# Performance work log

Hardware: AMD Instinct MI355X
Metric: run time of the kernel (lower is better)

Reference implementation:

```python
import jax, jax.numpy as jnp
from jax import lax
import numpy as np

NUM_TAGS = 64
B, T = 1024, 512


def setup_inputs() -> dict:
    key = jax.random.key(0)
    k1, k2, k3, k4, k5 = jax.random.split(key, 5)
    emissions = jax.random.normal(k1, (B, T, NUM_TAGS), dtype=jnp.float32)
    mask = jnp.ones((B, T), dtype=bool)
    tags = jax.random.randint(k2, (B, T), 0, NUM_TAGS, dtype=jnp.int32)
    # torch init: uniform(-0.1, 0.1)
    start_transitions = jax.random.uniform(k3, (NUM_TAGS,), jnp.float32, -0.1, 0.1)
    transitions = jax.random.uniform(k4, (NUM_TAGS, NUM_TAGS), jnp.float32, -0.1, 0.1)
    end_transitions = jax.random.uniform(k5, (NUM_TAGS,), jnp.float32, -0.1, 0.1)
    return {
        "emissions": emissions,
        "mask": mask,
        "tags": tags,
        "start_transitions": start_transitions,
        "transitions": transitions,
        "end_transitions": end_transitions,
    }


def _crf_nll(emissions, mask, tags, start_transitions, transitions, end_transitions):
    # emissions [B,T,K], mask [B,T] bool, tags [B,T] int
    em = jnp.moveaxis(emissions, 1, 0)        # [T,B,K]
    msk = jnp.moveaxis(mask, 1, 0)            # [T,B]
    tg = jnp.moveaxis(tags, 1, 0)             # [T,B]

    alpha0 = start_transitions[None, :] + em[0]   # [B,K]

    # ---- log-partition: logsumexp forward recursion ----
    def step_z(alpha, inp):
        e_t, m_t = inp
        # sum over previous tag i: alpha[b,i] + transitions[i,j]
        res = jax.nn.logsumexp(alpha[:, :, None] + transitions[None, :, :], axis=1)
        alpha = jnp.where(m_t[:, None], res + e_t, alpha)
        return alpha, None

    alphaT, _ = lax.scan(step_z, alpha0, (em[1:], msk[1:]))
    z = jax.nn.logsumexp(alphaT + end_transitions[None, :], axis=-1)  # [B]

    # ---- posterior (gold-path) potential recursion ----
    def step_p(beta, inp):
        e_t, m_t, prev_tag = inp
        prev_score = jnp.take_along_axis(beta, prev_tag[:, None], axis=1)  # [B,1]
        res = transitions[prev_tag] + prev_score                           # [B,K]
        beta = jnp.where(m_t[:, None], res + e_t, beta)
        return beta, None

    betaT, _ = lax.scan(step_p, alpha0, (em[1:], msk[1:], tg[:-1]))
    last_idx = jnp.sum(mask, axis=1) - 1                                    # [B]
    tag_last = jnp.take_along_axis(tags, last_idx[:, None], axis=1)[:, 0]   # [B]
    path_score = (jnp.take_along_axis(betaT, tag_last[:, None], axis=1)[:, 0]
                  + end_transitions[tag_last])                               # [B]

    nll = path_score - z
    return jnp.mean(nll)  # reduction='mean'


def reference(emissions, mask, tags, start_transitions, transitions, end_transitions):
    return _crf_nll(emissions, mask, tags, start_transitions, transitions, end_transitions)
```

## Files before the change

### kernel.cpp

```cpp
#include <hip/hip_runtime.h>


#define KTAGS 64
#define TSEQ 512
#define BATCH 1024
#define WPB 4

__global__ __launch_bounds__(256, 1) void crf_nll_kernel(
    const float* __restrict__ emissions,
    const int*   __restrict__ tags,
    const float* __restrict__ start_t,
    const float* __restrict__ trans,
    const float* __restrict__ end_t,
    float* __restrict__ out)
{
    __shared__ float trans_lds[KTAGS * KTAGS];
    __shared__ __align__(16) float q_lds[WPB][KTAGS];
    __shared__ int tags_lds[WPB][TSEQ];

    const int tid  = threadIdx.x;
    const int lane = tid & 63;
    const int wid  = tid >> 6;
    const int b    = blockIdx.x * WPB + wid;

    for (int i = tid; i < KTAGS * KTAGS; i += 256) trans_lds[i] = trans[i];
    const int* tag_row = tags + b * TSEQ;
    for (int i = lane; i < TSEQ; i += 64) tags_lds[wid][i] = tag_row[i];
    __syncthreads();

    float Ereg[KTAGS];
#pragma unroll
    for (int i = 0; i < KTAGS; ++i) Ereg[i] = __expf(trans[i * KTAGS + lane]);

    const float* em_row = emissions + (size_t)b * TSEQ * KTAGS;

    float e0     = em_row[lane];
    float alpha0 = start_t[lane] + e0;
    float beta   = alpha0;
    float c      = __shfl(alpha0, 0);
    float C      = c;
    float q      = __expf(alpha0 - c);
    q_lds[wid][lane] = q;

    float e_cur = em_row[1 * KTAGS + lane];
    float e_nxt = em_row[2 * KTAGS + lane];
    float pf0   = em_row[3 * KTAGS + lane];
    float pf1   = em_row[4 * KTAGS + lane];
    float pf2   = em_row[5 * KTAGS + lane];
    float e0c   = __shfl(e_cur, 0);
    float wc    = __expf(e_cur - e0c);

#pragma unroll 4
    for (int t = 1; t < TSEQ; ++t) {
        int   idx   = t + 5 < TSEQ ? t + 5 : TSEQ - 1;
        float e_new = em_row[idx * KTAGS + lane];

        float e0n = __shfl(e_nxt, 0);
        float wn  = __expf(e_nxt - e0n);

        const float4* pv4 = (const float4*)q_lds[wid];
        float4 qv[KTAGS / 4];
#pragma unroll
        for (int i = 0; i < KTAGS / 4; ++i) qv[i] = pv4[i];

        float a0 = 0.f, a1 = 0.f, a2 = 0.f, a3 = 0.f;
#pragma unroll
        for (int i = 0; i < KTAGS / 4; ++i) {
            a0 = fmaf(qv[i].x, Ereg[4 * i + 0], a0);
            a1 = fmaf(qv[i].y, Ereg[4 * i + 1], a1);
            a2 = fmaf(qv[i].z, Ereg[4 * i + 2], a2);
            a3 = fmaf(qv[i].w, Ereg[4 * i + 3], a3);
        }
        float s = (a0 + a1) + (a2 + a3);

        float sf   = __shfl(s, 0);
        float rinv = __builtin_amdgcn_rcpf(sf);
        C += __logf(sf) + e0c;
        q = s * rinv * wc;

        int   pt = tags_lds[wid][t - 1];
        float bp = __shfl(beta, pt);
        beta = trans_lds[pt * KTAGS + lane] + bp + e_cur;

        q_lds[wid][lane] = q;

        e_cur = e_nxt; e0c = e0n; wc = wn;
        e_nxt = pf0; pf0 = pf1; pf1 = pf2; pf2 = e_new;
    }

    float v  = q * __expf(end_t[lane]);
    float se = v;
#pragma unroll
    for (int off = 32; off > 0; off >>= 1) se += __shfl_xor(se, off);
    float z = C + __logf(se);

    int   tl   = tags_lds[wid][TSEQ - 1];
    float bl   = __shfl(beta, tl);
    float path = bl + end_t[tl];

    if (lane == 0) atomicAdd(out, (path - z) * (1.0f / BATCH));
}

extern "C" void kernel_launch(void* const* d_in, const int* in_sizes, int n_in,
                              void* d_out, int out_size, void* d_ws, size_t ws_size,
                              hipStream_t stream) {
    const float* emissions = (const float*)d_in[0];
    const int*   tags      = (const int*)d_in[2];
    const float* start_t   = (const float*)d_in[3];
    const float* trans     = (const float*)d_in[4];
    const float* end_t     = (const float*)d_in[5];
    float* out = (float*)d_out;

    hipMemsetAsync(out, 0, sizeof(float), stream);

    dim3 grid(BATCH / WPB);
    dim3 block(WPB * 64);
    crf_nll_kernel<<<grid, block, 0, stream>>>(emissions, tags, start_t, trans,
                                               end_t, out);
}
```

Measured before the change: 351.2 us.

## Normalize CRF forward recursion every fourth step and pipeline LDS loads

```diff
diff --git a/kernel.cpp b/kernel.cpp
--- a/kernel.cpp
+++ b/kernel.cpp
@@ -6,7 +6,15 @@
 #define BATCH 1024
 #define WPB 4
 
-__global__ __launch_bounds__(256, 1) void crf_nll_kernel(
+typedef float f4 __attribute__((ext_vector_type(4)));
+
+__device__ __forceinline__ float readlane0(float v) {
+    return __uint_as_float(__builtin_amdgcn_readlane(__float_as_uint(v), 0));
+}
+
+__global__ __launch_bounds__(256)
+__attribute__((amdgpu_waves_per_eu(1, 1)))
+void crf_nll_kernel(
     const float* __restrict__ emissions,
     const int*   __restrict__ tags,
     const float* __restrict__ start_t,
@@ -28,16 +36,25 @@
     for (int i = lane; i < TSEQ; i += 64) tags_lds[wid][i] = tag_row[i];
     __syncthreads();
 
-    float Ereg[KTAGS];
-#pragma unroll
-    for (int i = 0; i < KTAGS; ++i) Ereg[i] = __expf(trans[i * KTAGS + lane]);
+#define MKE(n) (f4){ __expf(trans_lds[(4*(n)+0)*KTAGS+lane]), \
+                     __expf(trans_lds[(4*(n)+1)*KTAGS+lane]), \
+                     __expf(trans_lds[(4*(n)+2)*KTAGS+lane]), \
+                     __expf(trans_lds[(4*(n)+3)*KTAGS+lane]) }
+    f4 E0 = MKE(0),  E1 = MKE(1),  E2 = MKE(2),  E3 = MKE(3),
+       E4 = MKE(4),  E5 = MKE(5),  E6 = MKE(6),  E7 = MKE(7),
+       E8 = MKE(8),  E9 = MKE(9),  E10 = MKE(10), E11 = MKE(11),
+       E12 = MKE(12), E13 = MKE(13), E14 = MKE(14), E15 = MKE(15);
+    asm volatile("" : "+v"(E0), "+v"(E1), "+v"(E2), "+v"(E3),
+                      "+v"(E4), "+v"(E5), "+v"(E6), "+v"(E7));
+    asm volatile("" : "+v"(E8), "+v"(E9), "+v"(E10), "+v"(E11),
+                      "+v"(E12), "+v"(E13), "+v"(E14), "+v"(E15));
 
     const float* em_row = emissions + (size_t)b * TSEQ * KTAGS;
 
-    float e0     = em_row[lane];
-    float alpha0 = start_t[lane] + e0;
+    float e0v    = em_row[lane];
+    float alpha0 = start_t[lane] + e0v;
     float beta   = alpha0;
-    float c      = __shfl(alpha0, 0);
+    float c      = readlane0(alpha0);
     float C      = c;
     float q      = __expf(alpha0 - c);
     q_lds[wid][lane] = q;
@@ -47,46 +64,69 @@
     float pf0   = em_row[3 * KTAGS + lane];
     float pf1   = em_row[4 * KTAGS + lane];
     float pf2   = em_row[5 * KTAGS + lane];
-    float e0c   = __shfl(e_cur, 0);
+    float e0c   = readlane0(e_cur);
     float wc    = __expf(e_cur - e0c);
 
-#pragma unroll 4
-    for (int t = 1; t < TSEQ; ++t) {
-        int   idx   = t + 5 < TSEQ ? t + 5 : TSEQ - 1;
-        float e_new = em_row[idx * KTAGS + lane];
+    int   pt_cur  = tags_lds[wid][0];
+    float trw_cur = trans_lds[pt_cur * KTAGS + lane];
 
-        float e0n = __shfl(e_nxt, 0);
-        float wn  = __expf(e_nxt - e0n);
+#define FMA4(qv, Ev, w0, w1, w2, w3)                                   \
+    w0 = fmaf((qv).x, (Ev).x, w0); w1 = fmaf((qv).y, (Ev).y, w1);      \
+    w2 = fmaf((qv).z, (Ev).z, w2); w3 = fmaf((qv).w, (Ev).w, w3);
 
-        const float4* pv4 = (const float4*)q_lds[wid];
-        float4 qv[KTAGS / 4];
-#pragma unroll
-        for (int i = 0; i < KTAGS / 4; ++i) qv[i] = pv4[i];
+#define STEP(t, DO_NORM) do {                                          \
+    int   idx   = (t) + 5 < TSEQ ? (t) + 5 : TSEQ - 1;                 \
+    float e_new = em_row[idx * KTAGS + lane];                          \
+    int   pt_nxt  = tags_lds[wid][(t)];                                \
+    float trw_nxt = trans_lds[pt_nxt * KTAGS + lane];                  \
+    float e0n = readlane0(e_nxt);                                      \
+    float wn  = __expf(e_nxt - e0n);                                   \
+    const f4* pv4 = (const f4*)q_lds[wid];                             \
+    float a0 = 0.f, a1 = 0.f, a2 = 0.f, a3 = 0.f;                      \
+    float a4 = 0.f, a5 = 0.f, a6 = 0.f, a7 = 0.f;                      \
+    f4 qa = pv4[0], qb = pv4[1], qc = pv4[2], qd = pv4[3];             \
+    FMA4(qa, E0,  a0,a1,a2,a3)  qa = pv4[4];                           \
+    FMA4(qb, E1,  a4,a5,a6,a7)  qb = pv4[5];                           \
+    FMA4(qc, E2,  a0,a1,a2,a3)  qc = pv4[6];                           \
+    FMA4(qd, E3,  a4,a5,a6,a7)  qd = pv4[7];                           \
+    FMA4(qa, E4,  a0,a1,a2,a3)  qa = pv4[8];                           \
+    FMA4(qb, E5,  a4,a5,a6,a7)  qb = pv4[9];                           \
+    FMA4(qc, E6,  a0,a1,a2,a3)  qc = pv4[10];                          \
+    FMA4(qd, E7,  a4,a5,a6,a7)  qd = pv4[11];                          \
+    FMA4(qa, E8,  a0,a1,a2,a3)  qa = pv4[12];                          \
+    FMA4(qb, E9,  a4,a5,a6,a7)  qb = pv4[13];                          \
+    FMA4(qc, E10, a0,a1,a2,a3)  qc = pv4[14];                          \
+    FMA4(qd, E11, a4,a5,a6,a7)  qd = pv4[15];                          \
+    FMA4(qa, E12, a0,a1,a2,a3)                                         \
+    FMA4(qb, E13, a4,a5,a6,a7)                                         \
+    FMA4(qc, E14, a0,a1,a2,a3)                                         \
+    FMA4(qd, E15, a4,a5,a6,a7)                                         \
+    float s = ((a0 + a1) + (a2 + a3)) + ((a4 + a5) + (a6 + a7));       \
+    if (DO_NORM) {                                                     \
+        float sf = readlane0(s);         \
+        C += __logf(sf) + e0c;                                         \
+        q = s * __builtin_amdgcn_rcpf(sf) * wc;                        \
+    } else {                                                           \
+        C += e0c;                                                      \
+        q = s * wc;                                                    \
+    }                                                                  \
+    float bp = __shfl(beta, pt_cur);                                   \
+    beta = trw_cur + bp + e_cur;                                       \
+    q_lds[wid][lane] = q;                                              \
+    e_cur = e_nxt; e0c = e0n; wc = wn;                                 \
+    e_nxt = pf0; pf0 = pf1; pf1 = pf2; pf2 = e_new;                    \
+    pt_cur = pt_nxt; trw_cur = trw_nxt;                                \
+} while (0)
 
-        float a0 = 0.f, a1 = 0.f, a2 = 0.f, a3 = 0.f;
-#pragma unroll
-        for (int i = 0; i < KTAGS / 4; ++i) {
-            a0 = fmaf(qv[i].x, Ereg[4 * i + 0], a0);
-            a1 = fmaf(qv[i].y, Ereg[4 * i + 1], a1);
-            a2 = fmaf(qv[i].z, Ereg[4 * i + 2], a2);
-            a3 = fmaf(qv[i].w, Ereg[4 * i + 3], a3);
-        }
-        float s = (a0 + a1) + (a2 + a3);
-
-        float sf   = __shfl(s, 0);
-        float rinv = __builtin_amdgcn_rcpf(sf);
-        C += __logf(sf) + e0c;
-        q = s * rinv * wc;
-
-        int   pt = tags_lds[wid][t - 1];
-        float bp = __shfl(beta, pt);
-        beta = trans_lds[pt * KTAGS + lane] + bp + e_cur;
-
-        q_lds[wid][lane] = q;
-
-        e_cur = e_nxt; e0c = e0n; wc = wn;
-        e_nxt = pf0; pf0 = pf1; pf1 = pf2; pf2 = e_new;
+    for (int tb = 1; tb + 3 < TSEQ; tb += 4) {
+        STEP(tb + 0, false);
+        STEP(tb + 1, false);
+        STEP(tb + 2, false);
+        STEP(tb + 3, true);
     }
+    STEP(509, false);
+    STEP(510, false);
+    STEP(511, true);
 
     float v  = q * __expf(end_t[lane]);
     float se = v;
```

Result: faster. 332.8 us (-5.2%).

## Split CRF partition into forward and backward halves with DPP matvec

Applied to the files above, without the earlier changes.

```diff
diff --git a/kernel.cpp b/kernel.cpp
--- a/kernel.cpp
+++ b/kernel.cpp
@@ -2,103 +2,224 @@
 
 
 #define KTAGS 64
-#define TSEQ 512
+#define TSEQ  512
 #define BATCH 1024
-#define WPB 4
-
-__global__ __launch_bounds__(256, 1) void crf_nll_kernel(
+#define WPB   4
+#define NBLK_DIR 256
+#define TSPLIT 255
+
+#define WS_QF   0
+#define WS_QB   (WS_QF + BATCH*KTAGS)
+#define WS_CF   (WS_QB + BATCH*KTAGS)
+#define WS_CB   (WS_CF + BATCH)
+#define WS_PATH (WS_CB + BATCH)
+
+__device__ __forceinline__ float readlane0(float v) {
+    return __uint_as_float(__builtin_amdgcn_readlane(__float_as_uint(v), 0));
+}
+__device__ __forceinline__ float bperm(int addr4, float v) {
+    return __uint_as_float(__builtin_amdgcn_ds_bpermute(addr4, __float_as_uint(v)));
+}
+
+#define FOR16(M, b) M(b,0) M(b,1) M(b,2) M(b,3) M(b,4) M(b,5) M(b,6) M(b,7) \
+                    M(b,8) M(b,9) M(b,10) M(b,11) M(b,12) M(b,13) M(b,14) M(b,15)
+
+#define DECL_EDF(b,r) float Ed_##b##_##r = \
+    __expf(trans_lds[((16*(b) + (((lane&15)+16-(r))&15))<<6) + lane]);
+#define DECL_EDB(b,r) float Ed_##b##_##r = \
+    __expf(trans_lds[(lane<<6) + 16*(b) + (((lane&15)+16-(r))&15)]);
+#define PIN_ED(b,r) asm volatile("" : "+v"(Ed_##b##_##r));
+
+#define MAC(acc, qv, b, r) \
+    asm("v_fmac_f32 %0, %1, %2 row_ror:" #r " row_mask:0xf bank_mask:0xf" \
+        : "+v"(acc) : "v"(qv), "v"(Ed_##b##_##r));
+#define MULD(acc, qv, b, r) \
+    asm("v_mul_f32 %0, %1, %2 row_ror:" #r " row_mask:0xf bank_mask:0xf" \
+        : "=v"(acc) : "v"(qv), "v"(Ed_##b##_##r));
+#define MACR_EVEN(r) MAC(a0,qb0,0,r) MAC(a1,qb1,1,r) MAC(a2,qb2,2,r) MAC(a3,qb3,3,r)
+#define MACR_ODD(r)  MAC(a4,qb0,0,r) MAC(a5,qb1,1,r) MAC(a6,qb2,2,r) MAC(a7,qb3,3,r)
+
+#define MATVEC_BODY \
+    float a0 = qb0*Ed_0_0, a1 = qb1*Ed_1_0, a2 = qb2*Ed_2_0, a3 = qb3*Ed_3_0; \
+    float a4, a5, a6, a7; \
+    MULD(a4,qb0,0,1) MULD(a5,qb1,1,1) MULD(a6,qb2,2,1) MULD(a7,qb3,3,1) \
+    MACR_EVEN(2)  MACR_ODD(3)  MACR_EVEN(4)  MACR_ODD(5) \
+    MACR_EVEN(6)  MACR_ODD(7)  MACR_EVEN(8)  MACR_ODD(9) \
+    MACR_EVEN(10) MACR_ODD(11) MACR_EVEN(12) MACR_ODD(13) \
+    MACR_EVEN(14) MACR_ODD(15)
+
+__global__ __launch_bounds__(256)
+__attribute__((amdgpu_waves_per_eu(2, 2)))
+void crf_fb_kernel(
     const float* __restrict__ emissions,
     const int*   __restrict__ tags,
     const float* __restrict__ start_t,
     const float* __restrict__ trans,
     const float* __restrict__ end_t,
-    float* __restrict__ out)
+    float* __restrict__ wsf)
 {
     __shared__ float trans_lds[KTAGS * KTAGS];
-    __shared__ __align__(16) float q_lds[WPB][KTAGS];
     __shared__ int tags_lds[WPB][TSEQ];
 
     const int tid  = threadIdx.x;
     const int lane = tid & 63;
     const int wid  = tid >> 6;
-    const int b    = blockIdx.x * WPB + wid;
+    const int bid  = blockIdx.x;
+    const bool fwd = bid < NBLK_DIR;
+    const int b    = (fwd ? bid : bid - NBLK_DIR) * WPB + wid;
 
     for (int i = tid; i < KTAGS * KTAGS; i += 256) trans_lds[i] = trans[i];
     const int* tag_row = tags + b * TSEQ;
     for (int i = lane; i < TSEQ; i += 64) tags_lds[wid][i] = tag_row[i];
     __syncthreads();
 
-    float Ereg[KTAGS];
+    const float* em_row = emissions + (size_t)b * TSEQ * KTAGS;
+    const int l16 = lane & 15;
+    const int gib0 = l16 << 2, gib1 = (16 | l16) << 2,
+              gib2 = (32 | l16) << 2, gib3 = (48 | l16) << 2;
+
+    if (fwd) {
+        FOR16(DECL_EDF, 0) FOR16(DECL_EDF, 1) FOR16(DECL_EDF, 2) FOR16(DECL_EDF, 3)
+        FOR16(PIN_ED, 0) FOR16(PIN_ED, 1) FOR16(PIN_ED, 2) FOR16(PIN_ED, 3)
+
+        float e0v    = em_row[lane];
+        float alpha0 = start_t[lane] + e0v;
+        float c      = readlane0(alpha0);
+        float C      = c;
+        float q0     = __expf(alpha0 - c);
+        float qb0 = bperm(gib0, q0), qb1 = bperm(gib1, q0),
+              qb2 = bperm(gib2, q0), qb3 = bperm(gib3, q0);
+
+        float e1    = em_row[1 * KTAGS + lane];
+        float e0c   = readlane0(e1);
+        float Wc    = __expf(e1 - e0c);
+        float e_nxt = em_row[2 * KTAGS + lane];
+        float pf0   = em_row[3 * KTAGS + lane];
+        float pf1   = em_row[4 * KTAGS + lane];
+        float pf2   = em_row[5 * KTAGS + lane];
+        float qcur  = q0;
+
+#define FSTEP(t, DO_NORM) do {                                         \
+        int idx = (t) + 5; if (idx > TSPLIT) idx = TSPLIT;             \
+        float e_new = em_row[idx * KTAGS + lane];                      \
+        float e0n = readlane0(e_nxt);                                  \
+        float wn  = __expf(e_nxt - e0n);                               \
+        MATVEC_BODY                                                    \
+        float s = ((a0+a1)+(a2+a3)) + ((a4+a5)+(a6+a7));               \
+        float q = s * Wc;                                              \
+        qb0 = bperm(gib0, q); qb1 = bperm(gib1, q);                    \
+        qb2 = bperm(gib2, q); qb3 = bperm(gib3, q);                    \
+        C += e0c;                                                      \
+        if (DO_NORM) {                                                 \
+            float sf = readlane0(q);                                   \
+            C += __logf(sf);                                           \
+            wn *= __builtin_amdgcn_rcpf(sf);                           \
+        }                                                              \
+        qcur = q; Wc = wn; e0c = e0n;                                  \
+        e_nxt = pf0; pf0 = pf1; pf1 = pf2; pf2 = e_new;                \
+    } while (0)
+
+        for (int tb = 1; tb + 3 <= 252; tb += 4) {
+            FSTEP(tb + 0, false);
+            FSTEP(tb + 1, false);
+            FSTEP(tb + 2, false);
+            FSTEP(tb + 3, true);
+        }
+        FSTEP(253, false);
+        FSTEP(254, false);
+        FSTEP(255, false);
+
+        float sf = readlane0(qcur);
+        C += __logf(sf);
+        qcur *= __builtin_amdgcn_rcpf(sf);
+        wsf[WS_QF + b * KTAGS + lane] = qcur;
+
+        float ps = 0.f;
+        int tbase = lane * 8;
+        int gp = (lane == 0) ? 0 : tags_lds[wid][tbase - 1];
 #pragma unroll
-    for (int i = 0; i < KTAGS; ++i) Ereg[i] = __expf(trans[i * KTAGS + lane]);
-
-    const float* em_row = emissions + (size_t)b * TSEQ * KTAGS;
-
-    float e0     = em_row[lane];
-    float alpha0 = start_t[lane] + e0;
-    float beta   = alpha0;
-    float c      = __shfl(alpha0, 0);
-    float C      = c;
-    float q      = __expf(alpha0 - c);
-    q_lds[wid][lane] = q;
-
-    float e_cur = em_row[1 * KTAGS + lane];
-    float e_nxt = em_row[2 * KTAGS + lane];
-    float pf0   = em_row[3 * KTAGS + lane];
-    float pf1   = em_row[4 * KTAGS + lane];
-    float pf2   = em_row[5 * KTAGS + lane];
-    float e0c   = __shfl(e_cur, 0);
-    float wc    = __expf(e_cur - e0c);
-
-#pragma unroll 4
-    for (int t = 1; t < TSEQ; ++t) {
-        int   idx   = t + 5 < TSEQ ? t + 5 : TSEQ - 1;
-        float e_new = em_row[idx * KTAGS + lane];
-
-        float e0n = __shfl(e_nxt, 0);
-        float wn  = __expf(e_nxt - e0n);
-
-        const float4* pv4 = (const float4*)q_lds[wid];
-        float4 qv[KTAGS / 4];
+        for (int u = 0; u < 8; ++u) {
+            int t = tbase + u;
+            int g = tags_lds[wid][t];
+            ps += em_row[t * KTAGS + g];
+            if (t > 0) ps += trans_lds[gp * KTAGS + g];
+            gp = g;
+        }
+        if (lane == 0)  ps += start_t[tags_lds[wid][0]];
+        if (lane == 63) ps += end_t[tags_lds[wid][TSEQ - 1]];
 #pragma unroll
-        for (int i = 0; i < KTAGS / 4; ++i) qv[i] = pv4[i];
-
-        float a0 = 0.f, a1 = 0.f, a2 = 0.f, a3 = 0.f;
+        for (int off = 32; off; off >>= 1) ps += __shfl_xor(ps, off);
+
+        if (lane == 0) { wsf[WS_CF + b] = C; wsf[WS_PATH + b] = ps; }
+
+    } else {
+        FOR16(DECL_EDB, 0) FOR16(DECL_EDB, 1) FOR16(DECL_EDB, 2) FOR16(DECL_EDB, 3)
+        FOR16(PIN_ED, 0) FOR16(PIN_ED, 1) FOR16(PIN_ED, 2) FOR16(PIN_ED, 3)
+
+        float ev   = end_t[lane];
+        float end0 = readlane0(ev);
+        float C    = end0;
+        float bcur = __expf(ev - end0);
+
+        float e511  = em_row[511 * KTAGS + lane];
+        float e0c   = readlane0(e511);
+        float Wc    = __expf(e511 - e0c);
+        float e_nxt = em_row[510 * KTAGS + lane];
+        float pf0   = em_row[509 * KTAGS + lane];
+        float pf1   = em_row[508 * KTAGS + lane];
+        float pf2   = em_row[507 * KTAGS + lane];
+
+#define BSTEP(it, DO_NORM) do {                                        \
+        int idx = 511 - (it) - 5; if (idx < 256) idx = 256;            \
+        float e_new = em_row[idx * KTAGS + lane];                      \
+        float e0n = readlane0(e_nxt);                                  \
+        float wn  = __expf(e_nxt - e0n);                               \
+        float u = bcur * Wc;                                           \
+        float qb0 = bperm(gib0, u), qb1 = bperm(gib1, u),              \
+              qb2 = bperm(gib2, u), qb3 = bperm(gib3, u);              \
+        MATVEC_BODY                                                    \
+        bcur = ((a0+a1)+(a2+a3)) + ((a4+a5)+(a6+a7));                  \
+        C += e0c;                                                      \
+        if (DO_NORM) {                                                 \
+            float sf = readlane0(bcur);                                \
+            C += __logf(sf);                                           \
+            wn *= __builtin_amdgcn_rcpf(sf);                           \
+        }                                                              \
+        Wc = wn; e0c = e0n;                                            \
+        e_nxt = pf0; pf0 = pf1; pf1 = pf2; pf2 = e_new;                \
+    } while (0)
+
+        for (int itb = 0; itb + 3 <= 255; itb += 4) {
+            BSTEP(itb + 0, false);
+            BSTEP(itb + 1, false);
+            BSTEP(itb + 2, false);
+            BSTEP(itb + 3, true);
+        }
+
+        float sf = readlane0(bcur);
+        C += __logf(sf);
+        bcur *= __builtin_amdgcn_rcpf(sf);
+        wsf[WS_QB + b * KTAGS + lane] = bcur;
+        if (lane == 0) wsf[WS_CB + b] = C;
+    }
+}
+
+__global__ __launch_bounds__(256) void crf_combine_kernel(
+    const float* __restrict__ wsf, float* __restrict__ out)
+{
+    const int lane = threadIdx.x & 63;
+    const int wid  = threadIdx.x >> 6;
+    const int b    = blockIdx.x * WPB + wid;
+
+    float p = wsf[WS_QF + b * KTAGS + lane] * wsf[WS_QB + b * KTAGS + lane];
 #pragma unroll
-        for (int i = 0; i < KTAGS / 4; ++i) {
-            a0 = fmaf(qv[i].x, Ereg[4 * i + 0], a0);
-            a1 = fmaf(qv[i].y, Ereg[4 * i + 1], a1);
-            a2 = fmaf(qv[i].z, Ereg[4 * i + 2], a2);
-            a3 = fmaf(qv[i].w, Ereg[4 * i + 3], a3);
-        }
-        float s = (a0 + a1) + (a2 + a3);
-
-        float sf   = __shfl(s, 0);
-        float rinv = __builtin_amdgcn_rcpf(sf);
-        C += __logf(sf) + e0c;
-        q = s * rinv * wc;
-
-        int   pt = tags_lds[wid][t - 1];
-        float bp = __shfl(beta, pt);
-        beta = trans_lds[pt * KTAGS + lane] + bp + e_cur;
-
-        q_lds[wid][lane] = q;
-
-        e_cur = e_nxt; e0c = e0n; wc = wn;
-        e_nxt = pf0; pf0 = pf1; pf1 = pf2; pf2 = e_new;
+    for (int off = 32; off; off >>= 1) p += __shfl_xor(p, off);
+
+    if (lane == 0) {
+        float z   = wsf[WS_CF + b] + wsf[WS_CB + b] + __logf(p);
+        float nll = wsf[WS_PATH + b] - z;
+        atomicAdd(out, nll * (1.0f / BATCH));
     }
-
-    float v  = q * __expf(end_t[lane]);
-    float se = v;
-#pragma unroll
-    for (int off = 32; off > 0; off >>= 1) se += __shfl_xor(se, off);
-    float z = C + __logf(se);
-
-    int   tl   = tags_lds[wid][TSEQ - 1];
-    float bl   = __shfl(beta, tl);
-    float path = bl + end_t[tl];
-
-    if (lane == 0) atomicAdd(out, (path - z) * (1.0f / BATCH));
 }
 
 extern "C" void kernel_launch(void* const* d_in, const int* in_sizes, int n_in,
@@ -110,11 +231,11 @@
     const float* trans     = (const float*)d_in[4];
     const float* end_t     = (const float*)d_in[5];
     float* out = (float*)d_out;
+    float* wsf = (float*)d_ws;
 
     hipMemsetAsync(out, 0, sizeof(float), stream);
 
-    dim3 grid(BATCH / WPB);
-    dim3 block(WPB * 64);
-    crf_nll_kernel<<<grid, block, 0, stream>>>(emissions, tags, start_t, trans,
-                                               end_t, out);
-}
+    crf_fb_kernel<<<dim3(2 * NBLK_DIR), dim3(256), 0, stream>>>(
+        emissions, tags, start_t, trans, end_t, wsf);
+    crf_combine_kernel<<<dim3(BATCH / WPB), dim3(256), 0, stream>>>(wsf, out);
+}
```

New measurement: 282.7 us. 19.5% less time.
